# Performance work log

Measured on AMD Instinct MI355X. Metric: run time of the kernel, lower is better.

## Reference

```python
import jax, jax.numpy as jnp
import numpy as np

B, S, D = 1, 1024, 4096
NH, NKV, HD = 32, 8, 128
CACHE = 1024


def setup_inputs() -> dict:
    key = jax.random.key(0)
    ks = jax.random.split(key, 9)
    return {
        "hidden_states": jax.random.normal(ks[0], (B, S, D), jnp.float32),
        "freqs_cos": jax.random.uniform(ks[1], (S, HD // 2), jnp.float32),
        "freqs_sin": jax.random.uniform(ks[2], (S, HD // 2), jnp.float32),
        "atten_mask": jnp.zeros((S, CACHE + S), jnp.float32),
        "k_cache": jax.random.normal(ks[3], (B, NKV, HD, CACHE), jnp.float32),
        "v_cache": jax.random.normal(ks[4], (B, NKV, CACHE, HD), jnp.float32),
        "wq": jax.random.normal(ks[5], (NH, HD, D), jnp.float32) * 0.02,
        "wk": jax.random.normal(ks[6], (NKV, HD, D), jnp.float32) * 0.02,
        "wv": jax.random.normal(ks[7], (NKV, HD, D), jnp.float32) * 0.02,
        "wo": jax.random.normal(ks[8], (D, NH * HD), jnp.float32) * 0.02,
    }


def _rope(x, cos, sin):
    # x: [b, s, h, hd]; cos/sin: [s, hd//2]
    half = x.shape[-1] // 2
    xr, xi = x[..., :half], x[..., half:]
    c = cos[None, :, None, :]
    sn = sin[None, :, None, :]
    return jnp.concatenate([xr * c - xi * sn, xr * sn + xi * c], axis=-1)


def reference(hidden_states, freqs_cos, freqs_sin, atten_mask, k_cache, v_cache, wq, wk, wv, wo):
    b, s, d = hidden_states.shape
    nh, hd, _ = wq.shape
    nkv = wk.shape[0]
    g = nh // nkv  # query heads per KV head
    scale = float(hd) ** 0.5

    # projections (equivalent to per-head 1x1 convs)
    q = jnp.einsum("bsd,hed->bshe", hidden_states, wq)   # [b,s,nh,hd]
    k = jnp.einsum("bsd,hed->bshe", hidden_states, wk)   # [b,s,nkv,hd]
    v = jnp.einsum("bsd,hed->bshe", hidden_states, wv)   # [b,s,nkv,hd]

    q = _rope(q, freqs_cos, freqs_sin)
    k = _rope(k, freqs_cos, freqs_sin)

    # concat KV cache: kh [b,nkv,hd,KV], vh [b,nkv,KV,hd]
    kh = jnp.concatenate([k_cache, k.transpose(0, 2, 3, 1)], axis=-1)
    vh = jnp.concatenate([v_cache, v.transpose(0, 2, 1, 3)], axis=2)

    # grouped attention: head i uses kv group i // g
    qg = q.reshape(b, s, nkv, g, hd).transpose(0, 2, 3, 1, 4)  # [b,n,g,s,e]
    scores = jnp.einsum("bngse,bnet->bngst", qg, kh) / scale + atten_mask
    p = jax.nn.softmax(scores, axis=-1)
    yg = jnp.einsum("bngst,bnte->bngse", p, vh)               # [b,n,g,s,e]
    y = yg.transpose(0, 3, 1, 2, 4).reshape(b, s, nh * hd)     # head order n*g+j

    y = jnp.einsum("bsf,df->bsd", y, wo)
    return (y, kh, vh)
```

## Files before the change

kernel.cpp:

```cpp
#include <hip/hip_runtime.h>
#include <hip/hip_bf16.h>
#include <stdint.h>

#define S_LEN 1024
#define D_MODEL 4096
#define NHEAD 32
#define NKV 8
#define HD 128
#define CACHE_T 1024
#define T_TOT 2048
#define NQKV 6144

typedef __attribute__((ext_vector_type(8))) short short8;
typedef __attribute__((ext_vector_type(4))) float floatx4;

__device__ __forceinline__ unsigned short f2bf(float f) {
  union { float f; uint32_t u; } v; v.f = f;
  uint32_t r = v.u + 0x7FFFu + ((v.u >> 16) & 1u);
  return (unsigned short)(r >> 16);
}

__device__ __forceinline__ void gload_lds16(const void* g, void* s) {
  __builtin_amdgcn_global_load_lds((const __attribute__((address_space(1))) void*)g,
                                   (__attribute__((address_space(3))) void*)s, 16, 0, 0);
}

__global__ void convf2b_kernel(const float* __restrict__ in, unsigned short* __restrict__ out, int n8) {
  int stride = gridDim.x * blockDim.x;
  for (int t = blockIdx.x * blockDim.x + threadIdx.x; t < n8; t += stride) {
    int i = t * 8;
    floatx4 a = *(const floatx4*)(in + i);
    floatx4 b = *(const floatx4*)(in + i + 4);
    short8 o;
    o[0] = (short)f2bf(a[0]); o[1] = (short)f2bf(a[1]); o[2] = (short)f2bf(a[2]); o[3] = (short)f2bf(a[3]);
    o[4] = (short)f2bf(b[0]); o[5] = (short)f2bf(b[1]); o[6] = (short)f2bf(b[2]); o[7] = (short)f2bf(b[3]);
    *(short8*)(out + i) = o;
  }
}

__global__ void mask_flag_kernel(const float* __restrict__ m, int n, int* __restrict__ flag) {
  int stride = gridDim.x * blockDim.x;
  bool nz = false;
  for (int i = blockIdx.x * blockDim.x + threadIdx.x; i < n; i += stride)
    nz |= (m[i] != 0.0f);
  if (nz) atomicOr(flag, 1);
}

__global__ __launch_bounds__(256, 3)
void gemm_bf_kernel(const unsigned short* __restrict__ A,
                    const unsigned short* __restrict__ W,
                    float* __restrict__ C,
                    int M, int N, int K, int ldc, int GM)
{
  __shared__ __align__(16) unsigned char As[2][64 * 128];
  __shared__ __align__(16) unsigned char Bs[2][128 * 128];

  const int nwg = gridDim.x;
  int orig = blockIdx.x;
  int wg = (orig & 7) * (nwg >> 3) + (orig >> 3);
  const int mt = wg % GM, nt = wg / GM;
  const int m0 = mt * 64, n0 = nt * 128;

  const int tid = threadIdx.x;
  const int wid = tid >> 6, lane = tid & 63;
  const int g4 = lane >> 4, r16 = lane & 15;
  const int wr = (wid >> 1) * 32, wc = (wid & 1) * 64;

  const int lr = lane >> 3, lc = lane & 7;
  const unsigned short* Arow[2];
  const unsigned short* Wrow[4];
#pragma unroll
  for (int i = 0; i < 2; ++i) {
    int r = (wid * 2 + i) * 8 + lr;
    Arow[i] = A + (size_t)(m0 + r) * K + (lc ^ (r & 7)) * 8;
  }
#pragma unroll
  for (int i = 0; i < 4; ++i) {
    int r = (wid * 4 + i) * 8 + lr;
    Wrow[i] = W + (size_t)(n0 + r) * K + (lc ^ (r & 7)) * 8;
  }

  auto stage = [&](int buf, int kt) {
    const int kb = kt * 64;
#pragma unroll
    for (int i = 0; i < 2; ++i)
      gload_lds16(Arow[i] + kb, &As[buf][(wid * 2 + i) * 1024]);
#pragma unroll
    for (int i = 0; i < 4; ++i)
      gload_lds16(Wrow[i] + kb, &Bs[buf][(wid * 4 + i) * 1024]);
  };

  floatx4 acc[2][4];
#pragma unroll
  for (int m = 0; m < 2; ++m)
#pragma unroll
    for (int n = 0; n < 4; ++n) acc[m][n] = (floatx4){0.f, 0.f, 0.f, 0.f};

  const int NK = K >> 6;
  stage(0, 0);
  __syncthreads();
  int cur = 0;
  for (int kt = 0; kt < NK; ++kt) {
    if (kt + 1 < NK) stage(cur ^ 1, kt + 1);
#pragma unroll
    for (int kk = 0; kk < 2; ++kk) {
      const int kb = kk * 64 + g4 * 16;
      short8 af[2], bf[4];
#pragma unroll
      for (int m = 0; m < 2; ++m) {
        int row = wr + m * 16 + r16;
        af[m] = *(const short8*)(&As[cur][row * 128 + (kb ^ ((row & 7) << 4))]);
      }
#pragma unroll
      for (int n = 0; n < 4; ++n) {
        int row = wc + n * 16 + r16;
        bf[n] = *(const short8*)(&Bs[cur][row * 128 + (kb ^ ((row & 7) << 4))]);
      }
#pragma unroll
      for (int m = 0; m < 2; ++m)
#pragma unroll
        for (int n = 0; n < 4; ++n)
          acc[m][n] = __builtin_amdgcn_mfma_f32_16x16x32_bf16(af[m], bf[n], acc[m][n], 0, 0, 0);
    }
    __syncthreads();
    cur ^= 1;
  }

#pragma unroll
  for (int m = 0; m < 2; ++m)
#pragma unroll
    for (int n = 0; n < 4; ++n)
#pragma unroll
      for (int j = 0; j < 4; ++j)
        C[(size_t)(m0 + wr + m * 16 + g4 * 4 + j) * ldc + (n0 + wc + n * 16 + r16)] = acc[m][n][j];
}

__global__ __launch_bounds__(256, 2)
void gemm_kernel(const unsigned short* __restrict__ A,
                 const float* __restrict__ W0, const float* __restrict__ W1, const float* __restrict__ W2,
                 int n1, int n2,
                 float* __restrict__ C,
                 int M, int N, int K, int GM)
{
  __shared__ __align__(16) unsigned char As[2][128 * 128];
  __shared__ __align__(16) unsigned char Bs[2][128 * 128];

  const int nwg = gridDim.x;
  int orig = blockIdx.x;
  int xcd = orig & 7, loc = orig >> 3;
  int q = nwg >> 3, r = nwg & 7;
  int wg = (xcd < r ? xcd * (q + 1) : r * (q + 1) + (xcd - r) * q) + loc;
  const int mt = wg % GM, nt = wg / GM;
  const int m0 = mt * 128, n0 = nt * 128;

  const int tid = threadIdx.x;
  const int wid = tid >> 6, lane = tid & 63;
  const int g4 = lane >> 4, r16 = lane & 15;
  const int wr = (wid >> 1) * 64, wc = (wid & 1) * 64;

  int srow[4], skc[4];
  const float* wptr[4];
#pragma unroll
  for (int i = 0; i < 4; ++i) {
    int c = tid + 256 * i;
    srow[i] = c >> 3; skc[i] = c & 7;
    int ng = n0 + srow[i];
    wptr[i] = (ng < n1) ? (W0 + (size_t)ng * K)
            : (ng < n2) ? (W1 + (size_t)(ng - n1) * K)
                        : (W2 + (size_t)(ng - n2) * K);
  }

  short8 ar[4]; floatx4 br[8];
  auto load_tile = [&](int kt) {
    int kb = kt * 64;
#pragma unroll
    for (int i = 0; i < 4; ++i) {
      ar[i] = *(const short8*)(A + (size_t)(m0 + srow[i]) * K + kb + skc[i] * 8);
      br[2 * i]     = *(const floatx4*)(wptr[i] + kb + skc[i] * 8);
      br[2 * i + 1] = *(const floatx4*)(wptr[i] + kb + skc[i] * 8 + 4);
    }
  };
  auto write_tile = [&](int buf) {
#pragma unroll
    for (int i = 0; i < 4; ++i) {
      int off = srow[i] * 128 + ((skc[i] * 16) ^ ((srow[i] & 7) << 4));
      *(short8*)(&As[buf][off]) = ar[i];
      short8 bb;
      bb[0] = (short)f2bf(br[2 * i][0]);     bb[1] = (short)f2bf(br[2 * i][1]);
      bb[2] = (short)f2bf(br[2 * i][2]);     bb[3] = (short)f2bf(br[2 * i][3]);
      bb[4] = (short)f2bf(br[2 * i + 1][0]); bb[5] = (short)f2bf(br[2 * i + 1][1]);
      bb[6] = (short)f2bf(br[2 * i + 1][2]); bb[7] = (short)f2bf(br[2 * i + 1][3]);
      *(short8*)(&Bs[buf][off]) = bb;
    }
  };

  floatx4 acc[4][4];
#pragma unroll
  for (int m = 0; m < 4; ++m)
#pragma unroll
    for (int n = 0; n < 4; ++n) acc[m][n] = (floatx4){0.f, 0.f, 0.f, 0.f};

  const int NK = K >> 6;
  load_tile(0);
  write_tile(0);
  __syncthreads();
  int cur = 0;
  for (int kt = 0; kt < NK; ++kt) {
    if (kt + 1 < NK) load_tile(kt + 1);
#pragma unroll
    for (int kk = 0; kk < 2; ++kk) {
      const int kb = kk * 32 + g4 * 8;
      short8 af[4], bfr[4];
#pragma unroll
      for (int m = 0; m < 4; ++m) {
        int row = wr + m * 16 + r16;
        af[m] = *(const short8*)(&As[cur][row * 128 + ((kb * 2) ^ ((row & 7) << 4))]);
      }
#pragma unroll
      for (int n = 0; n < 4; ++n) {
        int row = wc + n * 16 + r16;
        bfr[n] = *(const short8*)(&Bs[cur][row * 128 + ((kb * 2) ^ ((row & 7) << 4))]);
      }
#pragma unroll
      for (int m = 0; m < 4; ++m)
#pragma unroll
        for (int n = 0; n < 4; ++n)
          acc[m][n] = __builtin_amdgcn_mfma_f32_16x16x32_bf16(af[m], bfr[n], acc[m][n], 0, 0, 0);
    }
    if (kt + 1 < NK) write_tile(cur ^ 1);
    __syncthreads();
    cur ^= 1;
  }

#pragma unroll
  for (int m = 0; m < 4; ++m)
#pragma unroll
    for (int n = 0; n < 4; ++n)
#pragma unroll
      for (int j = 0; j < 4; ++j)
        C[(size_t)(m0 + wr + m * 16 + g4 * 4 + j) * N + (n0 + wc + n * 16 + r16)] = acc[m][n][j];
}

__global__ void rope_q_kernel(const float* __restrict__ qkv, const float* __restrict__ fc,
                              const float* __restrict__ fs, unsigned short* __restrict__ qb)
{
  const int s = blockIdx.x, t = threadIdx.x;
  const int head = t >> 3, e0 = (t & 7) * 8;
  const float* base = qkv + (size_t)s * NQKV + head * HD + e0;
  floatx4 xr0 = *(const floatx4*)(base);
  floatx4 xr1 = *(const floatx4*)(base + 4);
  floatx4 xi0 = *(const floatx4*)(base + 64);
  floatx4 xi1 = *(const floatx4*)(base + 68);
  floatx4 c0 = *(const floatx4*)(fc + s * 64 + e0);
  floatx4 c1 = *(const floatx4*)(fc + s * 64 + e0 + 4);
  floatx4 s0 = *(const floatx4*)(fs + s * 64 + e0);
  floatx4 s1 = *(const floatx4*)(fs + s * 64 + e0 + 4);
  short8 outr, outi;
#pragma unroll
  for (int j = 0; j < 4; ++j) {
    outr[j]     = (short)f2bf(xr0[j] * c0[j] - xi0[j] * s0[j]);
    outr[4 + j] = (short)f2bf(xr1[j] * c1[j] - xi1[j] * s1[j]);
    outi[j]     = (short)f2bf(xr0[j] * s0[j] + xi0[j] * c0[j]);
    outi[4 + j] = (short)f2bf(xr1[j] * s1[j] + xi1[j] * c1[j]);
  }
  unsigned short* ob = qb + (size_t)s * D_MODEL + head * HD + e0;
  *(short8*)ob = outr;
  *(short8*)(ob + 64) = outi;
}

__global__ void rope_k_kernel(const float* __restrict__ qkv, const float* __restrict__ fc,
                              const float* __restrict__ fs, float* __restrict__ kh,
                              unsigned short* __restrict__ khb)
{
  __shared__ float T[128][65];
  const int n = blockIdx.x >> 4, s0 = (blockIdx.x & 15) * 64;
  const int tid = threadIdx.x;
  const int sl = tid >> 2, e0 = (tid & 3) * 16;
  const int s = s0 + sl;
  const float* base = qkv + (size_t)s * NQKV + D_MODEL + n * HD;
  float xr[16], xi[16], cc[16], sn[16];
#pragma unroll
  for (int i = 0; i < 16; i += 4) {
    *(floatx4*)(xr + i) = *(const floatx4*)(base + e0 + i);
    *(floatx4*)(xi + i) = *(const floatx4*)(base + 64 + e0 + i);
    *(floatx4*)(cc + i) = *(const floatx4*)(fc + s * 64 + e0 + i);
    *(floatx4*)(sn + i) = *(const floatx4*)(fs + s * 64 + e0 + i);
  }
  short8 r0, r1, i0, i1;
#pragma unroll
  for (int i = 0; i < 16; ++i) {
    float vr = xr[i] * cc[i] - xi[i] * sn[i];
    float vi = xr[i] * sn[i] + xi[i] * cc[i];
    T[e0 + i][sl] = vr;
    T[64 + e0 + i][sl] = vi;
    unsigned short br = f2bf(vr), bi = f2bf(vi);
    if (i < 8) { r0[i] = (short)br; i0[i] = (short)bi; }
    else       { r1[i - 8] = (short)br; i1[i - 8] = (short)bi; }
  }
  unsigned short* kb = khb + ((size_t)n * T_TOT + CACHE_T + s) * HD;
  *(short8*)(kb + e0) = r0;       *(short8*)(kb + e0 + 8) = r1;
  *(short8*)(kb + 64 + e0) = i0;  *(short8*)(kb + 64 + e0 + 8) = i1;
  __syncthreads();
  const int e = tid >> 1, hf = tid & 1;
  float* dst = kh + ((size_t)n * HD + e) * T_TOT + CACHE_T + s0 + hf * 32;
#pragma unroll
  for (int i = 0; i < 32; i += 4) {
    floatx4 v;
    v[0] = T[e][hf * 32 + i]; v[1] = T[e][hf * 32 + i + 1];
    v[2] = T[e][hf * 32 + i + 2]; v[3] = T[e][hf * 32 + i + 3];
    *(floatx4*)(dst + i) = v;
  }
}

__global__ void v_scatter_kernel(const float* __restrict__ qkv, float* __restrict__ vh,
                                 unsigned short* __restrict__ vtb)
{
  __shared__ __align__(16) unsigned short T[128][72];
  const int n = blockIdx.x >> 4, s0 = (blockIdx.x & 15) * 64;
  const int tid = threadIdx.x;
  const int sl = tid >> 2, e0 = (tid & 3) * 32;
  const float* src = qkv + (size_t)(s0 + sl) * NQKV + D_MODEL + NKV * HD + n * HD + e0;
  float* dst = vh + ((size_t)n * T_TOT + CACHE_T + s0 + sl) * HD + e0;
#pragma unroll
  for (int i = 0; i < 32; i += 4) {
    floatx4 v = *(const floatx4*)(src + i);
    *(floatx4*)(dst + i) = v;
    T[e0 + i][sl] = f2bf(v[0]); T[e0 + i + 1][sl] = f2bf(v[1]);
    T[e0 + i + 2][sl] = f2bf(v[2]); T[e0 + i + 3][sl] = f2bf(v[3]);
  }
  __syncthreads();
  const int e = tid >> 1, hf = tid & 1;
  unsigned short* ob = vtb + ((size_t)n * HD + e) * T_TOT + CACHE_T + s0 + hf * 32;
#pragma unroll
  for (int i = 0; i < 32; i += 8) *(short8*)(ob + i) = *(const short8*)(&T[e][hf * 32 + i]);
}

__global__ void cache_k_kernel(const float* __restrict__ kc, float* __restrict__ kh,
                               unsigned short* __restrict__ khb)
{
  __shared__ __align__(16) unsigned short T[64][72];
  const int b = blockIdx.x;
  const int n = b >> 5, et = (b >> 4) & 1, tt = b & 15;
  const int e0 = et * 64, t0 = tt * 64;
  const int tid = threadIdx.x;
  const int el = tid >> 2, tc = (tid & 3) * 16;
  const float* src = kc + ((size_t)n * HD + e0 + el) * CACHE_T + t0 + tc;
  float* dst = kh + ((size_t)n * HD + e0 + el) * T_TOT + t0 + tc;
#pragma unroll
  for (int i = 0; i < 16; i += 4) {
    floatx4 v = *(const floatx4*)(src + i);
    *(floatx4*)(dst + i) = v;
    T[tc + i][el] = f2bf(v[0]); T[tc + i + 1][el] = f2bf(v[1]);
    T[tc + i + 2][el] = f2bf(v[2]); T[tc + i + 3][el] = f2bf(v[3]);
  }
  __syncthreads();
  const int tl = tid >> 2, ec = (tid & 3) * 16;
  unsigned short* ob = khb + ((size_t)n * T_TOT + t0 + tl) * HD + e0 + ec;
#pragma unroll
  for (int i = 0; i < 16; i += 8) *(short8*)(ob + i) = *(const short8*)(&T[tl][ec + i]);
}

__global__ void cache_v_kernel(const float* __restrict__ vc, float* __restrict__ vh,
                               unsigned short* __restrict__ vtb)
{
  __shared__ __align__(16) unsigned short T[128][72];
  const int n = blockIdx.x >> 4, t0 = (blockIdx.x & 15) * 64;
  const int tid = threadIdx.x;
  const int tl = tid >> 2, e0 = (tid & 3) * 32;
  const float* src = vc + ((size_t)n * CACHE_T + t0 + tl) * HD + e0;
  float* dst = vh + ((size_t)n * T_TOT + t0 + tl) * HD + e0;
#pragma unroll
  for (int i = 0; i < 32; i += 4) {
    floatx4 v = *(const floatx4*)(src + i);
    *(floatx4*)(dst + i) = v;
    T[e0 + i][tl] = f2bf(v[0]); T[e0 + i + 1][tl] = f2bf(v[1]);
    T[e0 + i + 2][tl] = f2bf(v[2]); T[e0 + i + 3][tl] = f2bf(v[3]);
  }
  __syncthreads();
  const int e = tid >> 1, hf = tid & 1;
  unsigned short* ob = vtb + ((size_t)n * HD + e) * T_TOT + t0 + hf * 32;
#pragma unroll
  for (int i = 0; i < 32; i += 8) *(short8*)(ob + i) = *(const short8*)(&T[e][hf * 32 + i]);
}

__global__ __launch_bounds__(256, 2)
void attn_kernel(const unsigned short* __restrict__ Qb, const unsigned short* __restrict__ Kb,
                 const unsigned short* __restrict__ Vb, const float* __restrict__ mask,
                 const int* __restrict__ flag, unsigned short* __restrict__ Ob)
{
  __shared__ __align__(16) unsigned char KL[64 * 256];
  __shared__ __align__(16) unsigned char VL[128 * 128];
  __shared__ __align__(16) unsigned short PL[4][16][72];

  int orig = blockIdx.x;
  int wg = (orig & 7) * 64 + (orig >> 3);
  const int nkv = wg >> 6;
  const int inner = wg & 63;
  const int h = nkv * 4 + (inner >> 4);
  const int qt = inner & 15;

  const int tid = threadIdx.x, wid = tid >> 6, lane = tid & 63;
  const int g4 = lane >> 4, r16 = lane & 15;
  const int srow = qt * 64 + wid * 16;
  const bool use_mask = (*flag) != 0;

  short8 qf[4];
#pragma unroll
  for (int ks = 0; ks < 4; ++ks)
    qf[ks] = *(const short8*)(Qb + (size_t)(srow + r16) * D_MODEL + h * HD + ks * 32 + g4 * 8);

  floatx4 acc[8];
#pragma unroll
  for (int fe = 0; fe < 8; ++fe) acc[fe] = (floatx4){0.f, 0.f, 0.f, 0.f};
  float mrow[4] = {-1e30f, -1e30f, -1e30f, -1e30f};
  float lrow[4] = {0.f, 0.f, 0.f, 0.f};

  const unsigned short* Kbase = Kb + (size_t)nkv * T_TOT * HD;
  const unsigned short* Vbase = Vb + (size_t)nkv * HD * T_TOT;
  const float sscale = 0.08838834764831845f;

  for (int t0 = 0; t0 < T_TOT; t0 += 64) {
#pragma unroll
    for (int i = 0; i < 4; ++i) {
      int c = tid + 256 * i, tr = c >> 4, ec = c & 15;
      short8 kv = *(const short8*)(Kbase + (size_t)(t0 + tr) * HD + ec * 8);
      *(short8*)(&KL[tr * 256 + ((ec * 16) ^ ((tr & 7) << 4))]) = kv;
    }
#pragma unroll
    for (int i = 0; i < 4; ++i) {
      int c = tid + 256 * i, er = c >> 3, tc = c & 7;
      short8 vv = *(const short8*)(Vbase + (size_t)er * T_TOT + t0 + tc * 8);
      *(short8*)(&VL[er * 128 + ((tc * 16) ^ ((er & 7) << 4))]) = vv;
    }
    __syncthreads();

    floatx4 sc[4];
#pragma unroll
    for (int fc4 = 0; fc4 < 4; ++fc4) {
      sc[fc4] = (floatx4){0.f, 0.f, 0.f, 0.f};
      const int trow = fc4 * 16 + r16;
#pragma unroll
      for (int ks = 0; ks < 4; ++ks) {
        short8 kf = *(const short8*)(&KL[trow * 256 + (((ks * 32 + g4 * 8) * 2) ^ ((trow & 7) << 4))]);
        sc[fc4] = __builtin_amdgcn_mfma_f32_16x16x32_bf16(qf[ks], kf, sc[fc4], 0, 0, 0);
      }
    }

    float sv[4][4];
#pragma unroll
    for (int fc4 = 0; fc4 < 4; ++fc4)
#pragma unroll
      for (int j = 0; j < 4; ++j) {
        float x = sc[fc4][j] * sscale;
        if (use_mask) x += mask[(size_t)(srow + g4 * 4 + j) * T_TOT + t0 + fc4 * 16 + r16];
        sv[fc4][j] = x;
      }

#pragma unroll
    for (int j = 0; j < 4; ++j) {
      float mx = fmaxf(fmaxf(sv[0][j], sv[1][j]), fmaxf(sv[2][j], sv[3][j]));
      mx = fmaxf(mx, __shfl_xor(mx, 1));
      mx = fmaxf(mx, __shfl_xor(mx, 2));
      mx = fmaxf(mx, __shfl_xor(mx, 4));
      mx = fmaxf(mx, __shfl_xor(mx, 8));
      float mn = fmaxf(mrow[j], mx);
      float corr = __expf(mrow[j] - mn);
      mrow[j] = mn;
      float ss = 0.f;
#pragma unroll
      for (int fc4 = 0; fc4 < 4; ++fc4) {
        float p = __expf(sv[fc4][j] - mn);
        sv[fc4][j] = p;
        ss += p;
      }
      ss += __shfl_xor(ss, 1); ss += __shfl_xor(ss, 2);
      ss += __shfl_xor(ss, 4); ss += __shfl_xor(ss, 8);
      lrow[j] = lrow[j] * corr + ss;
#pragma unroll
      for (int fe = 0; fe < 8; ++fe) acc[fe][j] *= corr;
    }

#pragma unroll
    for (int fc4 = 0; fc4 < 4; ++fc4)
#pragma unroll
      for (int j = 0; j < 4; ++j)
        PL[wid][g4 * 4 + j][fc4 * 16 + r16] = f2bf(sv[fc4][j]);
    __syncthreads();

    short8 pf[2];
#pragma unroll
    for (int ks = 0; ks < 2; ++ks)
      pf[ks] = *(const short8*)(&PL[wid][r16][ks * 32 + g4 * 8]);
#pragma unroll
    for (int fe = 0; fe < 8; ++fe) {
      const int erow = fe * 16 + r16;
#pragma unroll
      for (int ks = 0; ks < 2; ++ks) {
        short8 vf = *(const short8*)(&VL[erow * 128 + (((ks * 32 + g4 * 8) * 2) ^ ((erow & 7) << 4))]);
        acc[fe] = __builtin_amdgcn_mfma_f32_16x16x32_bf16(pf[ks], vf, acc[fe], 0, 0, 0);
      }
    }
    __syncthreads();
  }

#pragma unroll
  for (int j = 0; j < 4; ++j) {
    float inv = 1.0f / lrow[j];
    const size_t rowb = (size_t)(srow + g4 * 4 + j) * D_MODEL + h * HD;
#pragma unroll
    for (int fe = 0; fe < 8; ++fe)
      Ob[rowb + fe * 16 + r16] = f2bf(acc[fe][j] * inv);
  }
}

extern "C" void kernel_launch(void* const* d_in, const int* in_sizes, int n_in,
                              void* d_out, int out_size, void* d_ws, size_t ws_size,
                              hipStream_t stream)
{
  const float* hs   = (const float*)d_in[0];
  const float* fc   = (const float*)d_in[1];
  const float* fs   = (const float*)d_in[2];
  const float* mask = (const float*)d_in[3];
  const float* kc   = (const float*)d_in[4];
  const float* vc   = (const float*)d_in[5];
  const float* wq   = (const float*)d_in[6];
  const float* wk   = (const float*)d_in[7];
  const float* wv   = (const float*)d_in[8];
  const float* wo   = (const float*)d_in[9];

  float* y  = (float*)d_out;
  float* kh = y + (size_t)S_LEN * D_MODEL;
  float* vh = kh + (size_t)NKV * HD * T_TOT;

  char* ws = (char*)d_ws;
  unsigned short* hs_b   = (unsigned short*)ws;
  float* qkv             = (float*)(ws + 8388608u);
  unsigned short* attn_o = (unsigned short*)(ws + 8388608u);
  unsigned short* khb    = (unsigned short*)(ws + 33554432u);
  unsigned short* vtb    = (unsigned short*)(ws + 37748736u);
  int* flag              = (int*)(ws + 41943040u);
  unsigned short* slotW  = (unsigned short*)(ws + 41943296u);

  const size_t base = 41943296ull;
  const bool big = ws_size >= base + 50331648ull;
  const bool mid = ws_size >= base + 33554432ull;

  hipMemsetAsync(flag, 0, 4, stream);
  mask_flag_kernel<<<256, 256, 0, stream>>>(mask, S_LEN * T_TOT, flag);
  convf2b_kernel<<<2048, 256, 0, stream>>>(hs, hs_b, S_LEN * D_MODEL / 8);

  if (big) {
    convf2b_kernel<<<2048, 256, 0, stream>>>(wq, slotW, NHEAD * HD * D_MODEL / 8);
    convf2b_kernel<<<2048, 256, 0, stream>>>(wk, slotW + (size_t)4096 * 4096, NKV * HD * D_MODEL / 8);
    convf2b_kernel<<<2048, 256, 0, stream>>>(wv, slotW + (size_t)5120 * 4096, NKV * HD * D_MODEL / 8);
    gemm_bf_kernel<<<768, 256, 0, stream>>>(hs_b, slotW, qkv, 1024, 6144, 4096, 6144, 16);
  } else if (mid) {
    convf2b_kernel<<<2048, 256, 0, stream>>>(wk, slotW, NKV * HD * D_MODEL / 8);
    convf2b_kernel<<<2048, 256, 0, stream>>>(wv, slotW + (size_t)1024 * 4096, NKV * HD * D_MODEL / 8);
    gemm_bf_kernel<<<256, 256, 0, stream>>>(hs_b, slotW, qkv + 4096, 1024, 2048, 4096, 6144, 16);
    convf2b_kernel<<<2048, 256, 0, stream>>>(wq, slotW, NHEAD * HD * D_MODEL / 8);
    gemm_bf_kernel<<<512, 256, 0, stream>>>(hs_b, slotW, qkv, 1024, 4096, 4096, 6144, 16);
  } else {
    gemm_kernel<<<384, 256, 0, stream>>>(hs_b, wq, wk, wv, 4096, 5120, qkv, 1024, 6144, 4096, 8);
  }

  rope_q_kernel<<<1024, 256, 0, stream>>>(qkv, fc, fs, hs_b);
  rope_k_kernel<<<128, 256, 0, stream>>>(qkv, fc, fs, kh, khb);
  v_scatter_kernel<<<128, 256, 0, stream>>>(qkv, vh, vtb);
  cache_k_kernel<<<256, 256, 0, stream>>>(kc, kh, khb);
  cache_v_kernel<<<128, 256, 0, stream>>>(vc, vh, vtb);
  attn_kernel<<<512, 256, 0, stream>>>(hs_b, khb, vtb, mask, flag, attn_o);

  if (mid) {
    convf2b_kernel<<<2048, 256, 0, stream>>>(wo, slotW, D_MODEL * D_MODEL / 8);
    gemm_bf_kernel<<<512, 256, 0, stream>>>(attn_o, slotW, y, 1024, 4096, 4096, 4096, 16);
  } else {
    gemm_kernel<<<256, 256, 0, stream>>>(attn_o, wo, wo, wo, 1 << 29, 1 << 29, y, 1024, 4096, 4096, 8);
  }
}
```

Baseline: 288.7 us.

## Double-buffer K/V tiles via async global-to-LDS loads in attention kernel

The attention kernel now keeps two LDS buffers for the K and V tiles. It prefetches the next tile with global_load_lds while computing on the current one, which replaces the register round-trip load/store and the sync at the top of each iteration. The P scratch buffer drops its padding in favour of an XOR swizzle, and the sync between the P write and P read is removed because each wave only touches its own slice. This doubles K/V LDS use, which may reduce occupancy under the 2-blocks-per-CU bound. Correctness relies on the async loads completing before the single end-of-loop barrier.

```diff
diff --git a/kernel.cpp b/kernel.cpp
--- a/kernel.cpp
+++ b/kernel.cpp
@@ -388,9 +388,9 @@
                  const unsigned short* __restrict__ Vb, const float* __restrict__ mask,
                  const int* __restrict__ flag, unsigned short* __restrict__ Ob)
 {
-  __shared__ __align__(16) unsigned char KL[64 * 256];
-  __shared__ __align__(16) unsigned char VL[128 * 128];
-  __shared__ __align__(16) unsigned short PL[4][16][72];
+  __shared__ __align__(16) unsigned char KL[2][64 * 256];
+  __shared__ __align__(16) unsigned char VL[2][128 * 128];
+  __shared__ __align__(16) unsigned short PL[4][16][64];
 
   int orig = blockIdx.x;
   int wg = (orig & 7) * 64 + (orig >> 3);
@@ -419,20 +419,39 @@
   const unsigned short* Vbase = Vb + (size_t)nkv * HD * T_TOT;
   const float sscale = 0.08838834764831845f;
 
+  const unsigned short* kp[4];
+  const unsigned short* vp[4];
+  int kbase_off[4], vbase_off[4];
+#pragma unroll
+  for (int i = 0; i < 4; ++i) {
+    int krow = wid * 16 + i * 4 + (lane >> 4);
+    int kch  = (lane & 15) ^ (krow & 7);
+    kp[i] = Kbase + (size_t)krow * HD + kch * 8;
+    kbase_off[i] = (wid * 16 + i * 4) * 256;
+    int vrow = wid * 32 + i * 8 + (lane >> 3);
+    int vch  = (lane & 7) ^ (vrow & 7);
+    vp[i] = Vbase + (size_t)vrow * T_TOT + vch * 8;
+    vbase_off[i] = (wid * 32 + i * 8) * 128;
+  }
+
+#pragma unroll
+  for (int i = 0; i < 4; ++i) gload_lds16(kp[i], &KL[0][kbase_off[i]]);
+#pragma unroll
+  for (int i = 0; i < 4; ++i) gload_lds16(vp[i], &VL[0][vbase_off[i]]);
+#pragma unroll
+  for (int i = 0; i < 4; ++i) { kp[i] += 64 * HD; vp[i] += 64; }
+  __syncthreads();
+
+  int cur = 0;
   for (int t0 = 0; t0 < T_TOT; t0 += 64) {
-#pragma unroll
-    for (int i = 0; i < 4; ++i) {
-      int c = tid + 256 * i, tr = c >> 4, ec = c & 15;
-      short8 kv = *(const short8*)(Kbase + (size_t)(t0 + tr) * HD + ec * 8);
-      *(short8*)(&KL[tr * 256 + ((ec * 16) ^ ((tr & 7) << 4))]) = kv;
-    }
-#pragma unroll
-    for (int i = 0; i < 4; ++i) {
-      int c = tid + 256 * i, er = c >> 3, tc = c & 7;
-      short8 vv = *(const short8*)(Vbase + (size_t)er * T_TOT + t0 + tc * 8);
-      *(short8*)(&VL[er * 128 + ((tc * 16) ^ ((er & 7) << 4))]) = vv;
-    }
-    __syncthreads();
+    if (t0 + 64 < T_TOT) {
+#pragma unroll
+      for (int i = 0; i < 4; ++i) gload_lds16(kp[i], &KL[cur ^ 1][kbase_off[i]]);
+#pragma unroll
+      for (int i = 0; i < 4; ++i) gload_lds16(vp[i], &VL[cur ^ 1][vbase_off[i]]);
+#pragma unroll
+      for (int i = 0; i < 4; ++i) { kp[i] += 64 * HD; vp[i] += 64; }
+    }
 
     floatx4 sc[4];
 #pragma unroll
@@ -441,7 +460,7 @@
       const int trow = fc4 * 16 + r16;
 #pragma unroll
       for (int ks = 0; ks < 4; ++ks) {
-        short8 kf = *(const short8*)(&KL[trow * 256 + (((ks * 32 + g4 * 8) * 2) ^ ((trow & 7) << 4))]);
+        short8 kf = *(const short8*)(&KL[cur][trow * 256 + (((ks * 32 + g4 * 8) * 2) ^ ((trow & 7) << 4))]);
         sc[fc4] = __builtin_amdgcn_mfma_f32_16x16x32_bf16(qf[ks], kf, sc[fc4], 0, 0, 0);
       }
     }
@@ -483,24 +502,26 @@
 #pragma unroll
     for (int fc4 = 0; fc4 < 4; ++fc4)
 #pragma unroll
-      for (int j = 0; j < 4; ++j)
-        PL[wid][g4 * 4 + j][fc4 * 16 + r16] = f2bf(sv[fc4][j]);
-    __syncthreads();
+      for (int j = 0; j < 4; ++j) {
+        const int prow = g4 * 4 + j;
+        PL[wid][prow][(fc4 * 16 + r16) ^ ((prow & 7) << 3)] = f2bf(sv[fc4][j]);
+      }
 
     short8 pf[2];
 #pragma unroll
     for (int ks = 0; ks < 2; ++ks)
-      pf[ks] = *(const short8*)(&PL[wid][r16][ks * 32 + g4 * 8]);
+      pf[ks] = *(const short8*)(&PL[wid][r16][(ks * 32 + g4 * 8) ^ ((r16 & 7) << 3)]);
 #pragma unroll
     for (int fe = 0; fe < 8; ++fe) {
       const int erow = fe * 16 + r16;
 #pragma unroll
       for (int ks = 0; ks < 2; ++ks) {
-        short8 vf = *(const short8*)(&VL[erow * 128 + (((ks * 32 + g4 * 8) * 2) ^ ((erow & 7) << 4))]);
+        short8 vf = *(const short8*)(&VL[cur][erow * 128 + (((ks * 32 + g4 * 8) * 2) ^ ((erow & 7) << 4))]);
         acc[fe] = __builtin_amdgcn_mfma_f32_16x16x32_bf16(pf[ks], vf, acc[fe], 0, 0, 0);
       }
     }
     __syncthreads();
+    cur ^= 1;
   }
 
 #pragma unroll
```

Result: no change. 287.6 us (-0.4%).
